# Kernel tuning notes

Measured on AMD Instinct MI355X. Metric: run time of the kernel, lower is better.

The kernel has to match this reference:

```python
import jax, jax.numpy as jnp
import numpy as np

GAMMA = 10.0  # params[('edge_penalty_gamma', 10.0, ...)]
EPS_SQRT = 1e-24  # guard for sqrt(0) (float_aware_sqrt)


def dXf(u, dx):
    # forward difference along axis -2, Neumann-zero boundary (replicate last row)
    return (jnp.concatenate([u[..., 1:, :], u[..., -1:, :]], axis=-2) - u) / dx


def dYf(u, dy):
    # forward difference along axis -1, Neumann-zero boundary (replicate last col)
    return (jnp.concatenate([u[..., :, 1:], u[..., :, -1:]], axis=-1) - u) / dy


def setup_inputs() -> dict:
    key = jax.random.key(0)
    k1, k2 = jax.random.split(key)
    B, K, H, W = 8, 8, 1024, 1024
    input_images = jax.random.normal(k1, (B, 1, H, W), dtype=jnp.float32)
    spacing = jnp.ones((2,), dtype=jnp.float32)
    label_probabilities = jax.random.uniform(k2, (B, K, H, W), dtype=jnp.float32)
    return {"input_images": input_images, "spacing": spacing,
            "label_probabilities": label_probabilities}


def reference(input_images, spacing, label_probabilities):
    # --- compute_localized_edge_penalty(I, spacing) ---
    I = input_images[:, 0, ...]                      # [B, H, W]
    sx, sy = spacing[0], spacing[1]
    gn2 = dXf(I, sx) ** 2 + dYf(I, sy) ** 2          # ||grad I||^2 (forward diffs)
    gnI = jnp.sqrt(jnp.maximum(gn2, EPS_SQRT))
    w_edge = 1.0 / (1.0 + GAMMA * gnI * jnp.min(spacing))  # [B, H, W]

    # --- normalized-cut relaxation over all clusters, fully batched ---
    p = label_probabilities                          # [B, K, H, W]
    # cut-cost stencil uses unit spacing (fd.FD_torch(spacing=[1.0]*dim))
    p_xp = dXf(p, 1.0)
    p_yp = dYf(p, 1.0)
    w = w_edge[:, None, :, :]                        # broadcast over clusters
    nom = jnp.sum(p * (p + w * (p_xp + p_yp)), axis=(-2, -1))   # [B, K]
    denom = jnp.sum(p * (1.0 + 2.0 * w), axis=(-2, -1))         # [B, K]
    cut_cost = nom / denom                                        # [B, K]

    B, K = p.shape[0], p.shape[1]
    current_penalties = K - jnp.sum(cut_cost, axis=1)            # [B]
    return jnp.sum(current_penalties)
```

## Files before the change

### kernel.cpp

```cpp
#include <hip/hip_runtime.h>


constexpr int Bsz  = 8;
constexpr int Kc   = 8;
constexpr int H    = 1024;
constexpr int W    = 1024;
constexpr int ROWS = 8;
constexpr int RB   = H / ROWS;
constexpr int TPB  = 256;

#define GAMMA_F    10.0f
#define EPS_SQRT_F 1e-24f

__device__ __forceinline__ float wedge(float c, float dn, float rt,
                                       float inv_sx, float inv_sy, float smin) {
    float dx = (dn - c) * inv_sx;
    float dy = (rt - c) * inv_sy;
    float gn2 = dx * dx + dy * dy;
    float g = sqrtf(fmaxf(gn2, EPS_SQRT_F));
    return 1.0f / (1.0f + GAMMA_F * g * smin);
}

__device__ __forceinline__ void accum(float pc, float pd, float pr, float w,
                                      float& nom, float& den) {
    float lap = (pd - pc) + (pr - pc);
    nom = fmaf(pc, fmaf(w, lap, pc), nom);
    den = fmaf(pc, fmaf(2.0f, w, 1.0f), den);
}

__global__ __launch_bounds__(TPB) void cl_main(const float* __restrict__ I,
                                               const float* __restrict__ spacing,
                                               const float* __restrict__ P,
                                               float2* __restrict__ ws) {
    const int t  = threadIdx.x;
    const int j0 = t * 4;
    const int b  = blockIdx.y;
    const int r0 = blockIdx.x * ROWS;

    const float sx = spacing[0], sy = spacing[1];
    const float inv_sx = 1.0f / sx, inv_sy = 1.0f / sy;
    const float smin = fminf(sx, sy);

    const int jr = (j0 + 4 < W) ? (j0 + 4) : (W - 1);

    const float* Ib = I + (size_t)b * H * W;
    const float* Pb = P + (size_t)b * Kc * H * W;

    float nom[Kc], den[Kc];
#pragma unroll
    for (int k = 0; k < Kc; ++k) { nom[k] = 0.0f; den[k] = 0.0f; }

#pragma unroll 2
    for (int ii = 0; ii < ROWS; ++ii) {
        const int i = r0 + ii;
        const int inext = (i + 1 < H) ? (i + 1) : (H - 1);
        const size_t rc = (size_t)i * W;
        const size_t rn = (size_t)inext * W;

        const float4 cI  = *(const float4*)(Ib + rc + j0);
        const float4 nI  = *(const float4*)(Ib + rn + j0);
        const float  cIr = Ib[rc + jr];

        const float w0 = wedge(cI.x, nI.x, cI.y, inv_sx, inv_sy, smin);
        const float w1 = wedge(cI.y, nI.y, cI.z, inv_sx, inv_sy, smin);
        const float w2 = wedge(cI.z, nI.z, cI.w, inv_sx, inv_sy, smin);
        const float w3 = wedge(cI.w, nI.w, cIr,  inv_sx, inv_sy, smin);

#pragma unroll
        for (int k = 0; k < Kc; ++k) {
            const float* Pk = Pb + (size_t)k * H * W;
            const float4 cp  = *(const float4*)(Pk + rc + j0);
            const float4 np  = *(const float4*)(Pk + rn + j0);
            const float  cpr = Pk[rc + jr];

            accum(cp.x, np.x, cp.y, w0, nom[k], den[k]);
            accum(cp.y, np.y, cp.z, w1, nom[k], den[k]);
            accum(cp.z, np.z, cp.w, w2, nom[k], den[k]);
            accum(cp.w, np.w, cpr,  w3, nom[k], den[k]);
        }
    }

    __shared__ float red[4][2 * Kc];
    const int lane = t & 63;
    const int wave = t >> 6;

#pragma unroll
    for (int k = 0; k < Kc; ++k) {
        float n = nom[k], d = den[k];
#pragma unroll
        for (int off = 32; off > 0; off >>= 1) {
            n += __shfl_down(n, off, 64);
            d += __shfl_down(d, off, 64);
        }
        if (lane == 0) {
            red[wave][k]      = n;
            red[wave][Kc + k] = d;
        }
    }
    __syncthreads();

    if (t < Kc) {
        const int k = t;
        float n = red[0][k] + red[1][k] + red[2][k] + red[3][k];
        float d = red[0][Kc + k] + red[1][Kc + k] + red[2][Kc + k] + red[3][Kc + k];
        ws[((size_t)(b * RB + blockIdx.x)) * Kc + k] = make_float2(n, d);
    }
}

__global__ __launch_bounds__(512) void cl_final(const float2* __restrict__ ws,
                                                float* __restrict__ out) {
    const int t    = threadIdx.x;
    const int acc  = t & 63;
    const int part = t >> 6;
    const int b = acc >> 3, k = acc & 7;

    double n = 0.0, d = 0.0;
#pragma unroll
    for (int r = part; r < RB; r += 8) {
        const float2 v = ws[((size_t)(b * RB + r)) * Kc + k];
        n += (double)v.x;
        d += (double)v.y;
    }

    __shared__ double sn[64][8], sd[64][8];
    sn[acc][part] = n;
    sd[acc][part] = d;
    __syncthreads();

    if (t < 64) {
        double nn = 0.0, dd = 0.0;
#pragma unroll
        for (int p = 0; p < 8; ++p) { nn += sn[t][p]; dd += sd[t][p]; }
        double c = nn / dd;
#pragma unroll
        for (int off = 32; off > 0; off >>= 1) c += __shfl_down(c, off, 64);
        if (t == 0) out[0] = (float)((double)(Bsz * Kc) - c);
    }
}

extern "C" void kernel_launch(void* const* d_in, const int* in_sizes, int n_in,
                              void* d_out, int out_size, void* d_ws, size_t ws_size,
                              hipStream_t stream) {
    const float* I       = (const float*)d_in[0];
    const float* spacing = (const float*)d_in[1];
    const float* P       = (const float*)d_in[2];
    float* out = (float*)d_out;
    float2* ws = (float2*)d_ws;

    dim3 grid(RB, Bsz);
    cl_main<<<grid, TPB, 0, stream>>>(I, spacing, P, ws);
    cl_final<<<1, 512, 0, stream>>>(ws, out);
}
```

Measured before the change: 419.4 us.

## Roll current rows in registers, shuffle right neighbours, split clusters across grid z

Each thread now carries the current row of the image and probability tiles in registers and reuses the loaded next row as the following current row, so each row is fetched once rather than twice. The right-neighbour column comes from a wavefront shuffle, and only the last lane of each wave issues the scalar load. Clusters are split into two halves over a new grid z dimension, and rows per block double, so each block holds fewer accumulators. The image row and the edge weights are now computed twice, once per cluster half, and the loop is no longer unrolled.

```diff
diff --git a/kernel.cpp b/kernel.cpp
--- a/kernel.cpp
+++ b/kernel.cpp
@@ -3,9 +3,10 @@
 
 constexpr int Bsz  = 8;
 constexpr int Kc   = 8;
+constexpr int KPB  = 4;
 constexpr int H    = 1024;
 constexpr int W    = 1024;
-constexpr int ROWS = 8;
+constexpr int ROWS = 16;
 constexpr int RB   = H / ROWS;
 constexpr int TPB  = 256;
 
@@ -32,60 +33,81 @@
                                                const float* __restrict__ spacing,
                                                const float* __restrict__ P,
                                                float2* __restrict__ ws) {
-    const int t  = threadIdx.x;
-    const int j0 = t * 4;
-    const int b  = blockIdx.y;
-    const int r0 = blockIdx.x * ROWS;
+    const int t    = threadIdx.x;
+    const int lane = t & 63;
+    const int j0   = t * 4;
+    const int b    = blockIdx.y;
+    const int kh   = blockIdx.z;
+    const int r0   = blockIdx.x * ROWS;
 
     const float sx = spacing[0], sy = spacing[1];
     const float inv_sx = 1.0f / sx, inv_sy = 1.0f / sy;
     const float smin = fminf(sx, sy);
 
     const int jr = (j0 + 4 < W) ? (j0 + 4) : (W - 1);
+    const bool edge = (lane == 63);
 
     const float* Ib = I + (size_t)b * H * W;
-    const float* Pb = P + (size_t)b * Kc * H * W;
+    const float* Pk0 = P + ((size_t)(b * Kc + kh * KPB)) * H * W;
 
-    float nom[Kc], den[Kc];
+    float4 cI  = *(const float4*)(Ib + (size_t)r0 * W + j0);
+    float  cIr = edge ? Ib[(size_t)r0 * W + jr] : 0.0f;
+    float4 cp[KPB];
+    float  cpr[KPB];
 #pragma unroll
-    for (int k = 0; k < Kc; ++k) { nom[k] = 0.0f; den[k] = 0.0f; }
+    for (int k = 0; k < KPB; ++k) {
+        const float* Pk = Pk0 + (size_t)k * H * W;
+        cp[k]  = *(const float4*)(Pk + (size_t)r0 * W + j0);
+        cpr[k] = edge ? Pk[(size_t)r0 * W + jr] : 0.0f;
+    }
 
-#pragma unroll 2
+    float nom[KPB], den[KPB];
+#pragma unroll
+    for (int k = 0; k < KPB; ++k) { nom[k] = 0.0f; den[k] = 0.0f; }
+
+#pragma unroll 1
     for (int ii = 0; ii < ROWS; ++ii) {
         const int i = r0 + ii;
         const int inext = (i + 1 < H) ? (i + 1) : (H - 1);
-        const size_t rc = (size_t)i * W;
         const size_t rn = (size_t)inext * W;
 
-        const float4 cI  = *(const float4*)(Ib + rc + j0);
         const float4 nI  = *(const float4*)(Ib + rn + j0);
-        const float  cIr = Ib[rc + jr];
+        const float  nIr = edge ? Ib[rn + jr] : 0.0f;
+
+        float Irt = __shfl_down(cI.x, 1, 64);
+        if (edge) Irt = cIr;
 
         const float w0 = wedge(cI.x, nI.x, cI.y, inv_sx, inv_sy, smin);
         const float w1 = wedge(cI.y, nI.y, cI.z, inv_sx, inv_sy, smin);
         const float w2 = wedge(cI.z, nI.z, cI.w, inv_sx, inv_sy, smin);
-        const float w3 = wedge(cI.w, nI.w, cIr,  inv_sx, inv_sy, smin);
+        const float w3 = wedge(cI.w, nI.w, Irt,  inv_sx, inv_sy, smin);
 
 #pragma unroll
-        for (int k = 0; k < Kc; ++k) {
-            const float* Pk = Pb + (size_t)k * H * W;
-            const float4 cp  = *(const float4*)(Pk + rc + j0);
+        for (int k = 0; k < KPB; ++k) {
+            const float* Pk = Pk0 + (size_t)k * H * W;
             const float4 np  = *(const float4*)(Pk + rn + j0);
-            const float  cpr = Pk[rc + jr];
+            const float  npr = edge ? Pk[rn + jr] : 0.0f;
 
-            accum(cp.x, np.x, cp.y, w0, nom[k], den[k]);
-            accum(cp.y, np.y, cp.z, w1, nom[k], den[k]);
-            accum(cp.z, np.z, cp.w, w2, nom[k], den[k]);
-            accum(cp.w, np.w, cpr,  w3, nom[k], den[k]);
+            float prt = __shfl_down(cp[k].x, 1, 64);
+            if (edge) prt = cpr[k];
+
+            accum(cp[k].x, np.x, cp[k].y, w0, nom[k], den[k]);
+            accum(cp[k].y, np.y, cp[k].z, w1, nom[k], den[k]);
+            accum(cp[k].z, np.z, cp[k].w, w2, nom[k], den[k]);
+            accum(cp[k].w, np.w, prt,     w3, nom[k], den[k]);
+
+            cp[k]  = np;
+            cpr[k] = npr;
         }
+        cI  = nI;
+        cIr = nIr;
     }
 
-    __shared__ float red[4][2 * Kc];
-    const int lane = t & 63;
+    __shared__ float red[4][2 * KPB];
     const int wave = t >> 6;
 
 #pragma unroll
-    for (int k = 0; k < Kc; ++k) {
+    for (int k = 0; k < KPB; ++k) {
         float n = nom[k], d = den[k];
 #pragma unroll
         for (int off = 32; off > 0; off >>= 1) {
@@ -93,17 +115,17 @@
             d += __shfl_down(d, off, 64);
         }
         if (lane == 0) {
-            red[wave][k]      = n;
-            red[wave][Kc + k] = d;
+            red[wave][k]       = n;
+            red[wave][KPB + k] = d;
         }
     }
     __syncthreads();
 
-    if (t < Kc) {
+    if (t < KPB) {
         const int k = t;
         float n = red[0][k] + red[1][k] + red[2][k] + red[3][k];
-        float d = red[0][Kc + k] + red[1][Kc + k] + red[2][Kc + k] + red[3][Kc + k];
-        ws[((size_t)(b * RB + blockIdx.x)) * Kc + k] = make_float2(n, d);
+        float d = red[0][KPB + k] + red[1][KPB + k] + red[2][KPB + k] + red[3][KPB + k];
+        ws[(((size_t)(b * 2 + kh) * RB) + blockIdx.x) * KPB + k] = make_float2(n, d);
     }
 }
 
@@ -113,11 +135,12 @@
     const int acc  = t & 63;
     const int part = t >> 6;
     const int b = acc >> 3, k = acc & 7;
+    const int kh = k >> 2, kk = k & 3;
 
     double n = 0.0, d = 0.0;
 #pragma unroll
     for (int r = part; r < RB; r += 8) {
-        const float2 v = ws[((size_t)(b * RB + r)) * Kc + k];
+        const float2 v = ws[(((size_t)(b * 2 + kh) * RB) + r) * KPB + kk];
         n += (double)v.x;
         d += (double)v.y;
     }
@@ -147,7 +170,7 @@
     float* out = (float*)d_out;
     float2* ws = (float2*)d_ws;
 
-    dim3 grid(RB, Bsz);
+    dim3 grid(RB, Bsz, 2);
     cl_main<<<grid, TPB, 0, stream>>>(I, spacing, P, ws);
     cl_final<<<1, 512, 0, stream>>>(ws, out);
 }
```

New measurement: 385.2 us. 8.2% less time.
